# Optimization experiments

Hardware: AMD Instinct MI355X
Metric: run time of the kernel (lower is better)

## Reference

```python
import jax, jax.numpy as jnp
import numpy as np

NUM_HEADS = 12
EPS = 1e-6


def _rms_norm(x, w):
    # RMSNorm over the full channel dim (applied before head split), fp32 math
    return x * jax.lax.rsqrt(jnp.mean(x * x, axis=-1, keepdims=True) + EPS) * w


def _rope_apply(t, F, H, W, freqs):
    # t: [B, S, n, d] with S == F*H*W; freqs: [1024, d//2] angles
    B, S, n, d = t.shape
    c = d // 2
    s0 = c - 2 * (c // 3)  # temporal split (22 when d=128)
    s1 = c // 3            # spatial splits (21, 21)
    f0, f1, f2 = freqs[:, :s0], freqs[:, s0:s0 + s1], freqs[:, s0 + s1:]
    ang = jnp.concatenate([
        jnp.broadcast_to(f0[:F, None, None, :], (F, H, W, s0)),
        jnp.broadcast_to(f1[None, :H, None, :], (F, H, W, s1)),
        jnp.broadcast_to(f2[None, None, :W, :], (F, H, W, s1)),
    ], axis=-1).reshape(S, c)                      # [S, c]
    cos = jnp.cos(ang)[None, :, None, :]           # [1, S, 1, c]
    sin = jnp.sin(ang)[None, :, None, :]
    tp = t.reshape(B, S, n, c, 2)
    te, to = tp[..., 0], tp[..., 1]                # complex (real, imag) pairs
    rot = jnp.stack([te * cos - to * sin, te * sin + to * cos], axis=-1)
    return rot.reshape(B, S, n, d)


def reference(x, seq_lens, grid_sizes, freqs, Wq, bq, Wk, bk, Wv, bv, Wo, bo, norm_q_w, norm_k_w):
    B, S, C = x.shape
    n = NUM_HEADS
    d = C // n
    gs = np.asarray(grid_sizes)[0]
    F, H, W = int(gs[0]), int(gs[1]), int(gs[2])  # static: L == F*H*W, same per sample

    q = _rms_norm(x @ Wq.T + bq, norm_q_w).reshape(B, S, n, d)
    k = _rms_norm(x @ Wk.T + bk, norm_k_w).reshape(B, S, n, d)
    v = (x @ Wv.T + bv).reshape(B, S, n, d)

    q = _rope_apply(q, F, H, W, freqs)
    k = _rope_apply(k, F, H, W, freqs)

    scale = 1.0 / jnp.sqrt(jnp.float32(d))
    scores = jnp.einsum('bqnd,bknd->bnqk', q, k) * scale   # [B, n, S, S]
    kmask = jnp.arange(S)[None, :] < seq_lens[:, None]      # [B, S] valid keys
    scores = jnp.where(kmask[:, None, None, :], scores, -jnp.inf)
    attn = jax.nn.softmax(scores, axis=-1)
    out = jnp.einsum('bnqk,bknd->bqnd', attn, v).reshape(B, S, C)
    return out @ Wo.T + bo


def setup_inputs() -> dict:
    key = jax.random.key(0)
    ks = jax.random.split(key, 10)
    B, F, H, W = 2, 4, 24, 32
    S = F * H * W  # 3072
    C = 1536
    d = C // NUM_HEADS  # 128
    c = d // 2          # 64

    x = jax.random.normal(ks[0], (B, S, C), dtype=jnp.float32)
    seq_lens = jnp.array([S, 2500], dtype=jnp.int32)
    grid_sizes = jnp.array([[F, H, W]] * B, dtype=jnp.int32)

    # rope angles: outer(pos, 1/theta^(2i/dim)) per split [22, 21, 21]
    def rope_params(max_len, dim_k, theta=10000.0):
        inv = 1.0 / (theta ** (np.arange(0, dim_k, 2, dtype=np.float64) / dim_k))
        return np.outer(np.arange(max_len), inv)
    s0 = c - 2 * (c // 3)
    s1 = c // 3
    freqs = jnp.asarray(np.concatenate([
        rope_params(1024, 2 * s0), rope_params(1024, 2 * s1), rope_params(1024, 2 * s1)
    ], axis=1), dtype=jnp.float32)  # [1024, 64]

    std = 0.02
    def lin(k):
        return jax.random.normal(k, (C, C), dtype=jnp.float32) * std
    return {
        'x': x, 'seq_lens': seq_lens, 'grid_sizes': grid_sizes, 'freqs': freqs,
        'Wq': lin(ks[1]), 'bq': jnp.zeros((C,), jnp.float32),
        'Wk': lin(ks[2]), 'bk': jnp.zeros((C,), jnp.float32),
        'Wv': lin(ks[3]), 'bv': jnp.zeros((C,), jnp.float32),
        'Wo': lin(ks[4]), 'bo': jnp.zeros((C,), jnp.float32),
        'norm_q_w': jnp.ones((C,), jnp.float32),
        'norm_k_w': jnp.ones((C,), jnp.float32),
    }
```

## Files before the change

### kernel.cpp

```cpp
#include <hip/hip_runtime.h>
#include <hip/hip_bf16.h>
#include <math.h>

#define NB 2
#define SS 3072
#define CC 1536
#define NH 12
#define DH 128
#define NTOK (NB * SS)
#define WE (CC * CC)
#define LOG2E 1.4426950408889634f

typedef __attribute__((ext_vector_type(8))) short short8;
typedef __attribute__((ext_vector_type(4))) float floatx4;

#define GLOAD(g, l) __builtin_amdgcn_global_load_lds( \
    (const __attribute__((address_space(1))) void*)(g), \
    (__attribute__((address_space(3))) void*)(l), 16, 0, 0)

__device__ __forceinline__ unsigned short f2bf(float f) {
    unsigned u = __float_as_uint(f);
    u += 0x7fffu + ((u >> 16) & 1u);
    return (unsigned short)(u >> 16);
}
__device__ __forceinline__ int swz(int row, int q) {
    return row * 4 + (q ^ ((row >> 1) & 3));
}

__global__ __launch_bounds__(256) void cast_all(
    const float* __restrict__ x,
    const float* __restrict__ w0, const float* __restrict__ w1,
    const float* __restrict__ w2, const float* __restrict__ w3,
    unsigned short* __restrict__ o)
{
    const int y = blockIdx.y;
    const float* src = (y < 4) ? x + (size_t)y * WE
                     : (y == 4) ? w0 : (y == 5) ? w1 : (y == 6) ? w2 : w3;
    size_t i = ((size_t)blockIdx.x * 256 + threadIdx.x) * 4;
    float4 v = *(const float4*)&src[i];
    uint2 u;
    u.x = (unsigned)f2bf(v.x) | ((unsigned)f2bf(v.y) << 16);
    u.y = (unsigned)f2bf(v.z) | ((unsigned)f2bf(v.w) << 16);
    *(uint2*)&o[(size_t)y * WE + i] = u;
}

__global__ __launch_bounds__(256) void rope_table(
    const float* __restrict__ freqs, const int* __restrict__ gsz,
    float2* __restrict__ tab)
{
    const int id = blockIdx.x * 256 + threadIdx.x;
    const int s = id >> 6, pj = id & 63;
    const int Hg = gsz[1], Wg = gsz[2];
    const int f = s / (Hg * Wg);
    const int rem = s - f * Hg * Wg;
    const int hh = rem / Wg;
    const int ww = rem - hh * Wg;
    const int row = (pj < 22) ? f : ((pj < 43) ? hh : ww);
    float sn, cs;
    sincosf(freqs[row * 64 + pj], &sn, &cs);
    tab[id] = make_float2(cs, sn);
}

__global__ __launch_bounds__(256) void qkv_gemm(
    const unsigned short* __restrict__ X,
    const unsigned short* __restrict__ Wqb, const unsigned short* __restrict__ Wkb,
    const unsigned short* __restrict__ Wvb,
    const float* __restrict__ bq, const float* __restrict__ bk,
    const float* __restrict__ bv,
    unsigned short* __restrict__ qo, unsigned short* __restrict__ ko,
    unsigned short* __restrict__ vto)
{
    __shared__ unsigned short As[128 * 32];
    __shared__ unsigned short Bs[128 * 32];
    const int tid = threadIdx.x;
    const int w = tid >> 6, l = tid & 63;
    const int jseg = blockIdx.y / 12;
    const unsigned short* Wt = (jseg == 0) ? Wqb : (jseg == 1) ? Wkb : Wvb;
    const float* bias        = (jseg == 0) ? bq  : (jseg == 1) ? bk  : bv;
    unsigned short* Y        = (jseg == 0) ? qo  : (jseg == 1) ? ko  : vto;
    const int i0 = blockIdx.x * 128, j0 = (blockIdx.y % 12) * 128;
    const int srow = tid >> 2;
    const int gk8 = (((tid & 3) ^ ((srow >> 1) & 3))) * 8;

    floatx4 acc[4][4] = {};
    for (int k0 = 0; k0 < CC; k0 += 32) {
        __syncthreads();
        GLOAD(X + (size_t)(i0 + srow) * CC + k0 + gk8,        As + (size_t)tid * 8);
        GLOAD(X + (size_t)(i0 + 64 + srow) * CC + k0 + gk8,   As + (size_t)(256 + tid) * 8);
        GLOAD(Wt + (size_t)(j0 + srow) * CC + k0 + gk8,       Bs + (size_t)tid * 8);
        GLOAD(Wt + (size_t)(j0 + 64 + srow) * CC + k0 + gk8,  Bs + (size_t)(256 + tid) * 8);
        __syncthreads();
        const int wr = (w >> 1) * 64, wc = (w & 1) * 64;
        short8 af[4], bf[4];
        #pragma unroll
        for (int mb = 0; mb < 4; ++mb)
            af[mb] = *(const short8*)&As[swz(wr + mb * 16 + (l & 15), l >> 4) * 8];
        #pragma unroll
        for (int nb = 0; nb < 4; ++nb)
            bf[nb] = *(const short8*)&Bs[swz(wc + nb * 16 + (l & 15), l >> 4) * 8];
        #pragma unroll
        for (int mb = 0; mb < 4; ++mb)
            #pragma unroll
            for (int nb = 0; nb < 4; ++nb)
                acc[mb][nb] = __builtin_amdgcn_mfma_f32_16x16x32_bf16(
                    af[mb], bf[nb], acc[mb][nb], 0, 0, 0);
    }

    const int wr = (w >> 1) * 64, wc = (w & 1) * 64;
    #pragma unroll
    for (int mb = 0; mb < 4; ++mb)
        #pragma unroll
        for (int nb = 0; nb < 4; ++nb) {
            const int n = j0 + wc + nb * 16 + (l & 15);
            const float bv2 = bias[n];
            const int h = n >> 7, td = n & 127;
            #pragma unroll
            for (int r = 0; r < 4; ++r) {
                const int m = i0 + wr + mb * 16 + (l >> 4) * 4 + r;
                const float val = acc[mb][nb][r] + bv2;
                const int b = (m >= SS) ? 1 : 0;
                const int s = m - b * SS;
                if (jseg < 2)
                    Y[((size_t)(b * NH + h) * SS + s) * DH + td] = f2bf(val);
                else
                    Y[((size_t)(b * NH + h) * DH + td) * SS + s] = f2bf(val);
            }
        }
}

__global__ __launch_bounds__(256) void gemm_o(
    const unsigned short* __restrict__ X, const unsigned short* __restrict__ Wt,
    const float* __restrict__ bias, float* __restrict__ Y)
{
    __shared__ unsigned short As[128 * 32];
    __shared__ unsigned short Bs[128 * 32];
    const int tid = threadIdx.x;
    const int w = tid >> 6, l = tid & 63;
    const int i0 = blockIdx.x * 128, j0 = blockIdx.y * 128;
    const int srow = tid >> 2;
    const int gk8 = (((tid & 3) ^ ((srow >> 1) & 3))) * 8;

    floatx4 acc[4][4] = {};
    for (int k0 = 0; k0 < CC; k0 += 32) {
        __syncthreads();
        GLOAD(X + (size_t)(i0 + srow) * CC + k0 + gk8,        As + (size_t)tid * 8);
        GLOAD(X + (size_t)(i0 + 64 + srow) * CC + k0 + gk8,   As + (size_t)(256 + tid) * 8);
        GLOAD(Wt + (size_t)(j0 + srow) * CC + k0 + gk8,       Bs + (size_t)tid * 8);
        GLOAD(Wt + (size_t)(j0 + 64 + srow) * CC + k0 + gk8,  Bs + (size_t)(256 + tid) * 8);
        __syncthreads();
        const int wr = (w >> 1) * 64, wc = (w & 1) * 64;
        short8 af[4], bf[4];
        #pragma unroll
        for (int mb = 0; mb < 4; ++mb)
            af[mb] = *(const short8*)&As[swz(wr + mb * 16 + (l & 15), l >> 4) * 8];
        #pragma unroll
        for (int nb = 0; nb < 4; ++nb)
            bf[nb] = *(const short8*)&Bs[swz(wc + nb * 16 + (l & 15), l >> 4) * 8];
        #pragma unroll
        for (int mb = 0; mb < 4; ++mb)
            #pragma unroll
            for (int nb = 0; nb < 4; ++nb)
                acc[mb][nb] = __builtin_amdgcn_mfma_f32_16x16x32_bf16(
                    af[mb], bf[nb], acc[mb][nb], 0, 0, 0);
    }

    const int wr = (w >> 1) * 64, wc = (w & 1) * 64;
    #pragma unroll
    for (int mb = 0; mb < 4; ++mb)
        #pragma unroll
        for (int nb = 0; nb < 4; ++nb) {
            const int n = j0 + wc + nb * 16 + (l & 15);
            const float bv = bias[n];
            #pragma unroll
            for (int r = 0; r < 4; ++r) {
                const int m = i0 + wr + mb * 16 + (l >> 4) * 4 + r;
                Y[(size_t)m * CC + n] = acc[mb][nb][r] + bv;
            }
        }
}

__global__ __launch_bounds__(256) void norm_rope(
    unsigned short* __restrict__ qb, unsigned short* __restrict__ kb,
    const float* __restrict__ nqw, const float* __restrict__ nkw,
    const float2* __restrict__ tab)
{
    const int bid = blockIdx.x;
    const int which = (bid >= NTOK) ? 1 : 0;
    const int tok = bid - which * NTOK;
    unsigned short* t    = which ? kb : qb;
    const float* wgt     = which ? nkw : nqw;
    const float outscale = which ? 1.0f : 0.08838834764831845f * LOG2E;
    const int b = tok / SS, s = tok - b * SS;
    const int tid = threadIdx.x;

    float2 vals[3];
    size_t addrs[3];
    float ss = 0.f;
    #pragma unroll
    for (int kt = 0; kt < 3; ++kt) {
        int p = tid + kt * 256;
        int h = p >> 6, pj = p & 63;
        size_t addr = ((size_t)(b * NH + h) * SS + s) * DH + 2 * pj;
        addrs[kt] = addr;
        unsigned u = *(const unsigned*)&t[addr];
        float2 v;
        v.x = __uint_as_float(u << 16);
        v.y = __uint_as_float(u & 0xffff0000u);
        vals[kt] = v;
        ss += v.x * v.x + v.y * v.y;
    }
    #pragma unroll
    for (int off = 32; off > 0; off >>= 1) ss += __shfl_down(ss, off, 64);
    __shared__ float red[4];
    if ((tid & 63) == 0) red[tid >> 6] = ss;
    __syncthreads();
    const float total = red[0] + red[1] + red[2] + red[3];
    const float rstd = rsqrtf(total * (1.0f / CC) + 1e-6f) * outscale;

    #pragma unroll
    for (int kt = 0; kt < 3; ++kt) {
        int p = tid + kt * 256;
        int h = p >> 6, pj = p & 63;
        float2 cssn = tab[s * 64 + pj];
        int ch = h * DH + 2 * pj;
        float te = vals[kt].x * rstd * wgt[ch];
        float to = vals[kt].y * rstd * wgt[ch + 1];
        unsigned o = (unsigned)f2bf(te * cssn.x - to * cssn.y) |
                     ((unsigned)f2bf(te * cssn.y + to * cssn.x) << 16);
        *(unsigned*)&t[addrs[kt]] = o;
    }
}

__global__ __launch_bounds__(256, 2) void flash_attn_mfma(
    const unsigned short* __restrict__ qg, const unsigned short* __restrict__ kg,
    const unsigned short* __restrict__ vg, const int* __restrict__ seq_lens,
    unsigned short* __restrict__ out)
{
    __shared__ unsigned short lds[32768];
    const int tid = threadIdx.x;
    const int w = tid >> 6, l = tid & 63;

    const int bid = blockIdx.x;
    const int qt = bid / (NB * NH);
    const int rem0 = bid - qt * (NB * NH);
    const int h = rem0 >> 1;
    const int b = rem0 & 1;
    const int slen = seq_lens[b];
    const int s0 = qt * 128;

    const unsigned short* qbase = qg + ((size_t)(b * NH + h) * SS + s0) * DH;
    const unsigned short* kbase = kg + ((size_t)(b * NH + h) * SS) * DH;
    const unsigned short* vbase = vg + ((size_t)(b * NH + h) * DH) * SS;

    #pragma unroll
    for (int i = 0; i < 8; ++i) {
        int cid = i * 256 + tid;
        int kc = cid >> 9, r2 = cid & 511, row = r2 >> 2, sq = r2 & 3;
        GLOAD(qbase + (size_t)row * DH + kc * 32 + (sq ^ ((row >> 1) & 3)) * 8,
              lds + (size_t)cid * 8);
    }
    __syncthreads();
    short8 qf[2][4];
    #pragma unroll
    for (int rb = 0; rb < 2; ++rb)
        #pragma unroll
        for (int kc = 0; kc < 4; ++kc)
            qf[rb][kc] = *(const short8*)&lds[(kc * 512 + swz(w * 32 + rb * 16 + (l & 15), l >> 4)) * 8];
    __syncthreads();

    int ksrc[4], vsrc[4];
    #pragma unroll
    for (int i = 0; i < 4; ++i) {
        int cid = i * 256 + tid;
        {   int kc = cid >> 8, r2 = cid & 255, row = r2 >> 2, sq = r2 & 3;
            ksrc[i] = row * DH + kc * 32 + (sq ^ ((row >> 1) & 3)) * 8; }
        {   int ks = cid >> 9, r2 = cid & 511, dc = r2 >> 2, sq = r2 & 3;
            vsrc[i] = dc * SS + ks * 32 + (sq ^ ((dc >> 1) & 3)) * 8; }
    }

    const int ntiles = (slen + 63) >> 6;

    #pragma unroll
    for (int i = 0; i < 4; ++i) {
        int cid = i * 256 + tid;
        GLOAD(kbase + ksrc[i],        lds + (size_t)cid * 8);
        GLOAD(vbase + vsrc[i],        lds + 8192 + (size_t)cid * 8);
    }

    floatx4 acc[2][8] = {};
    float lsum[2] = {};
    const int g4 = (l >> 4) * 4;

    for (int kt = 0; kt < ntiles; ++kt) {
        __syncthreads();

        if (kt + 1 < ntiles) {
            const unsigned short* kb2 = kbase + (size_t)(kt + 1) * 64 * DH;
            const unsigned short* vb2 = vbase + (size_t)(kt + 1) * 64;
            unsigned short* dst = lds + ((kt + 1) & 1) * 16384;
            #pragma unroll
            for (int i = 0; i < 4; ++i) {
                int cid = i * 256 + tid;
                GLOAD(kb2 + ksrc[i], dst + (size_t)cid * 8);
                GLOAD(vb2 + vsrc[i], dst + 8192 + (size_t)cid * 8);
            }
        }

        const unsigned short* Ks = lds + (kt & 1) * 16384;
        const unsigned short* Vs = Ks + 8192;

        floatx4 sv[2][4] = {};
        __builtin_amdgcn_s_setprio(1);
        #pragma unroll
        for (int kc = 0; kc < 4; ++kc) {
            short8 kf[4];
            #pragma unroll
            for (int nb = 0; nb < 4; ++nb)
                kf[nb] = *(const short8*)&Ks[(kc * 256 + swz(nb * 16 + (l & 15), l >> 4)) * 8];
            #pragma unroll
            for (int rb = 0; rb < 2; ++rb)
                #pragma unroll
                for (int nb = 0; nb < 4; ++nb)
                    sv[rb][nb] = __builtin_amdgcn_mfma_f32_16x16x32_bf16(
                        kf[nb], qf[rb][kc], sv[rb][nb], 0, 0, 0);
        }
        __builtin_amdgcn_s_setprio(0);

        const int valid = slen - kt * 64;
        short8 pa[2][2];
        #pragma unroll
        for (int rb = 0; rb < 2; ++rb) {
            if (valid >= 64) {
                #pragma unroll
                for (int nb = 0; nb < 4; ++nb)
                    #pragma unroll
                    for (int r = 0; r < 4; ++r)
                        sv[rb][nb][r] = exp2f(sv[rb][nb][r]);
            } else {
                #pragma unroll
                for (int nb = 0; nb < 4; ++nb)
                    #pragma unroll
                    for (int r = 0; r < 4; ++r) {
                        const int key = g4 + r + 16 * nb;
                        sv[rb][nb][r] = (key < valid) ? exp2f(sv[rb][nb][r]) : 0.0f;
                    }
            }
            #pragma unroll
            for (int nb = 0; nb < 4; ++nb)
                lsum[rb] += (sv[rb][nb][0] + sv[rb][nb][1]) +
                            (sv[rb][nb][2] + sv[rb][nb][3]);

            unsigned dw0[4], dw1[4];
            #pragma unroll
            for (int nb = 0; nb < 4; ++nb) {
                union { __hip_bfloat162 v; unsigned u; } c0, c1;
                c0.v = __float22bfloat162_rn(make_float2(sv[rb][nb][0], sv[rb][nb][1]));
                c1.v = __float22bfloat162_rn(make_float2(sv[rb][nb][2], sv[rb][nb][3]));
                dw0[nb] = c0.u;
                dw1[nb] = c1.u;
            }
            #pragma unroll
            for (int ks = 0; ks < 2; ++ks) {
                unsigned x0 = dw0[2 * ks], y0 = dw0[2 * ks + 1];
                unsigned x1 = dw1[2 * ks], y1 = dw1[2 * ks + 1];
                asm("v_permlane32_swap_b32 %0, %1" : "+v"(x0), "+v"(y0));
                asm("v_permlane16_swap_b32 %0, %1" : "+v"(x0), "+v"(y0));
                asm("v_permlane32_swap_b32 %0, %1" : "+v"(x1), "+v"(y1));
                asm("v_permlane16_swap_b32 %0, %1" : "+v"(x1), "+v"(y1));
                union { short8 s; unsigned u[4]; } pk;
                pk.u[0] = x0; pk.u[1] = x1; pk.u[2] = y0; pk.u[3] = y1;
                pa[rb][ks] = pk.s;
            }
        }

        __builtin_amdgcn_s_setprio(1);
        #pragma unroll
        for (int ks = 0; ks < 2; ++ks)
            #pragma unroll
            for (int nb2 = 0; nb2 < 8; ++nb2) {
                short8 vf = *(const short8*)&Vs[(ks * 512 + swz(nb2 * 16 + (l & 15), l >> 4)) * 8];
                #pragma unroll
                for (int rb = 0; rb < 2; ++rb)
                    acc[rb][nb2] = __builtin_amdgcn_mfma_f32_16x16x32_bf16(
                        pa[rb][ks], vf, acc[rb][nb2], 0, 0, 0);
            }
        __builtin_amdgcn_s_setprio(0);
    }

    #pragma unroll
    for (int rb = 0; rb < 2; ++rb) {
        float s = lsum[rb];
        s += __shfl_xor(s, 16, 64);
        s += __shfl_xor(s, 32, 64);
        float rl[4];
        #pragma unroll
        for (int r = 0; r < 4; ++r)
            rl[r] = 1.0f / __shfl(s, g4 + r, 64);
        #pragma unroll
        for (int nb2 = 0; nb2 < 8; ++nb2) {
            const int col = h * DH + nb2 * 16 + (l & 15);
            #pragma unroll
            for (int r = 0; r < 4; ++r) {
                const int srow = s0 + w * 32 + rb * 16 + (l >> 4) * 4 + r;
                out[((size_t)b * SS + srow) * CC + col] = f2bf(acc[rb][nb2][r] * rl[r]);
            }
        }
    }
}

extern "C" void kernel_launch(void* const* d_in, const int* in_sizes, int n_in,
                              void* d_out, int out_size, void* d_ws, size_t ws_size,
                              hipStream_t stream) {
    const float* x          = (const float*)d_in[0];
    const int*   seq_lens   = (const int*)d_in[1];
    const int*   grid_sizes = (const int*)d_in[2];
    const float* freqs      = (const float*)d_in[3];
    const float* Wq         = (const float*)d_in[4];
    const float* bq         = (const float*)d_in[5];
    const float* Wk         = (const float*)d_in[6];
    const float* bk         = (const float*)d_in[7];
    const float* Wv         = (const float*)d_in[8];
    const float* bv         = (const float*)d_in[9];
    const float* Wo         = (const float*)d_in[10];
    const float* bo         = (const float*)d_in[11];
    const float* nqw        = (const float*)d_in[12];
    const float* nkw        = (const float*)d_in[13];
    float* out = (float*)d_out;

    const size_t TE = (size_t)NTOK * CC;
    unsigned short* xb  = (unsigned short*)d_ws;
    unsigned short* wqb = xb + TE;
    unsigned short* wkb = wqb + WE;
    unsigned short* wvb = wkb + WE;
    unsigned short* wob = wvb + WE;
    unsigned short* qb  = wob + WE;
    unsigned short* kb  = qb + TE;
    unsigned short* vtb = kb + TE;
    unsigned short* ab  = vtb + TE;
    float2* tab = (float2*)(ab + TE);

    cast_all<<<dim3(WE / 1024, 8), 256, 0, stream>>>(x, Wq, Wk, Wv, Wo, xb);
    rope_table<<<dim3(SS * 64 / 256), 256, 0, stream>>>(freqs, grid_sizes, tab);

    qkv_gemm<<<dim3(NTOK / 128, 36), 256, 0, stream>>>(
        xb, wqb, wkb, wvb, bq, bk, bv, qb, kb, vtb);

    norm_rope<<<dim3(2 * NTOK), 256, 0, stream>>>(qb, kb, nqw, nkw, tab);

    flash_attn_mfma<<<dim3(NB * NH * (SS / 128)), 256, 0, stream>>>(qb, kb, vtb, seq_lens, ab);

    gemm_o<<<dim3(NTOK / 128, CC / 128), 256, 0, stream>>>(ab, wob, bo, out);
}
```

Measured before the change: 519.1 us.

## Double-buffer GEMM LDS tiles and make flash attention a persistent work queue

Both GEMM kernels now double-buffer their LDS tiles. Each k-step prefetches the next tile with global_load_lds while it computes the current one, which drops one barrier per iteration. Flash attention becomes persistent: 512 blocks pull (q-tile, head, batch) items from an atomic counter that rope_table resets, which is meant to balance the uneven seq_len work. The trade-offs are more LDS per GEMM block, which may lower occupancy, plus atomic and barrier overhead per item. The GEMM prefetch also relies on the waitcnt before the single barrier for correctness.

```diff
diff --git a/kernel.cpp b/kernel.cpp
--- a/kernel.cpp
+++ b/kernel.cpp
@@ -10,6 +10,7 @@
 #define NTOK (NB * SS)
 #define WE (CC * CC)
 #define LOG2E 1.4426950408889634f
+#define NITEMS (NB * NH * (SS / 128))
 
 typedef __attribute__((ext_vector_type(8))) short short8;
 typedef __attribute__((ext_vector_type(4))) float floatx4;
@@ -46,9 +47,10 @@
 
 __global__ __launch_bounds__(256) void rope_table(
     const float* __restrict__ freqs, const int* __restrict__ gsz,
-    float2* __restrict__ tab)
+    float2* __restrict__ tab, int* __restrict__ ctr)
 {
     const int id = blockIdx.x * 256 + threadIdx.x;
+    if (id == 0) *ctr = 0;
     const int s = id >> 6, pj = id & 63;
     const int Hg = gsz[1], Wg = gsz[2];
     const int f = s / (Hg * Wg);
@@ -70,8 +72,8 @@
     unsigned short* __restrict__ qo, unsigned short* __restrict__ ko,
     unsigned short* __restrict__ vto)
 {
-    __shared__ unsigned short As[128 * 32];
-    __shared__ unsigned short Bs[128 * 32];
+    __shared__ unsigned short As[2 * 4096];
+    __shared__ unsigned short Bs[2 * 4096];
     const int tid = threadIdx.x;
     const int w = tid >> 6, l = tid & 63;
     const int jseg = blockIdx.y / 12;
@@ -82,28 +84,38 @@
     const int srow = tid >> 2;
     const int gk8 = (((tid & 3) ^ ((srow >> 1) & 3))) * 8;
 
+    GLOAD(X + (size_t)(i0 + srow) * CC + gk8,        As + (size_t)tid * 8);
+    GLOAD(X + (size_t)(i0 + 64 + srow) * CC + gk8,   As + (size_t)(256 + tid) * 8);
+    GLOAD(Wt + (size_t)(j0 + srow) * CC + gk8,       Bs + (size_t)tid * 8);
+    GLOAD(Wt + (size_t)(j0 + 64 + srow) * CC + gk8,  Bs + (size_t)(256 + tid) * 8);
+
     floatx4 acc[4][4] = {};
+    int cur = 0;
     for (int k0 = 0; k0 < CC; k0 += 32) {
         __syncthreads();
-        GLOAD(X + (size_t)(i0 + srow) * CC + k0 + gk8,        As + (size_t)tid * 8);
-        GLOAD(X + (size_t)(i0 + 64 + srow) * CC + k0 + gk8,   As + (size_t)(256 + tid) * 8);
-        GLOAD(Wt + (size_t)(j0 + srow) * CC + k0 + gk8,       Bs + (size_t)tid * 8);
-        GLOAD(Wt + (size_t)(j0 + 64 + srow) * CC + k0 + gk8,  Bs + (size_t)(256 + tid) * 8);
-        __syncthreads();
+        if (k0 + 32 < CC) {
+            const int nxt = (cur ^ 1) * 4096;
+            GLOAD(X + (size_t)(i0 + srow) * CC + k0 + 32 + gk8,        As + (size_t)(nxt + tid * 8));
+            GLOAD(X + (size_t)(i0 + 64 + srow) * CC + k0 + 32 + gk8,   As + (size_t)(nxt + (256 + tid) * 8));
+            GLOAD(Wt + (size_t)(j0 + srow) * CC + k0 + 32 + gk8,       Bs + (size_t)(nxt + tid * 8));
+            GLOAD(Wt + (size_t)(j0 + 64 + srow) * CC + k0 + 32 + gk8,  Bs + (size_t)(nxt + (256 + tid) * 8));
+        }
         const int wr = (w >> 1) * 64, wc = (w & 1) * 64;
+        const int cb = cur * 4096;
         short8 af[4], bf[4];
         #pragma unroll
         for (int mb = 0; mb < 4; ++mb)
-            af[mb] = *(const short8*)&As[swz(wr + mb * 16 + (l & 15), l >> 4) * 8];
+            af[mb] = *(const short8*)&As[cb + swz(wr + mb * 16 + (l & 15), l >> 4) * 8];
         #pragma unroll
         for (int nb = 0; nb < 4; ++nb)
-            bf[nb] = *(const short8*)&Bs[swz(wc + nb * 16 + (l & 15), l >> 4) * 8];
+            bf[nb] = *(const short8*)&Bs[cb + swz(wc + nb * 16 + (l & 15), l >> 4) * 8];
         #pragma unroll
         for (int mb = 0; mb < 4; ++mb)
             #pragma unroll
             for (int nb = 0; nb < 4; ++nb)
                 acc[mb][nb] = __builtin_amdgcn_mfma_f32_16x16x32_bf16(
                     af[mb], bf[nb], acc[mb][nb], 0, 0, 0);
+        cur ^= 1;
     }
 
     const int wr = (w >> 1) * 64, wc = (w & 1) * 64;
@@ -132,36 +144,46 @@
     const unsigned short* __restrict__ X, const unsigned short* __restrict__ Wt,
     const float* __restrict__ bias, float* __restrict__ Y)
 {
-    __shared__ unsigned short As[128 * 32];
-    __shared__ unsigned short Bs[128 * 32];
+    __shared__ unsigned short As[2 * 4096];
+    __shared__ unsigned short Bs[2 * 4096];
     const int tid = threadIdx.x;
     const int w = tid >> 6, l = tid & 63;
     const int i0 = blockIdx.x * 128, j0 = blockIdx.y * 128;
     const int srow = tid >> 2;
     const int gk8 = (((tid & 3) ^ ((srow >> 1) & 3))) * 8;
 
+    GLOAD(X + (size_t)(i0 + srow) * CC + gk8,        As + (size_t)tid * 8);
+    GLOAD(X + (size_t)(i0 + 64 + srow) * CC + gk8,   As + (size_t)(256 + tid) * 8);
+    GLOAD(Wt + (size_t)(j0 + srow) * CC + gk8,       Bs + (size_t)tid * 8);
+    GLOAD(Wt + (size_t)(j0 + 64 + srow) * CC + gk8,  Bs + (size_t)(256 + tid) * 8);
+
     floatx4 acc[4][4] = {};
+    int cur = 0;
     for (int k0 = 0; k0 < CC; k0 += 32) {
         __syncthreads();
-        GLOAD(X + (size_t)(i0 + srow) * CC + k0 + gk8,        As + (size_t)tid * 8);
-        GLOAD(X + (size_t)(i0 + 64 + srow) * CC + k0 + gk8,   As + (size_t)(256 + tid) * 8);
-        GLOAD(Wt + (size_t)(j0 + srow) * CC + k0 + gk8,       Bs + (size_t)tid * 8);
-        GLOAD(Wt + (size_t)(j0 + 64 + srow) * CC + k0 + gk8,  Bs + (size_t)(256 + tid) * 8);
-        __syncthreads();
+        if (k0 + 32 < CC) {
+            const int nxt = (cur ^ 1) * 4096;
+            GLOAD(X + (size_t)(i0 + srow) * CC + k0 + 32 + gk8,        As + (size_t)(nxt + tid * 8));
+            GLOAD(X + (size_t)(i0 + 64 + srow) * CC + k0 + 32 + gk8,   As + (size_t)(nxt + (256 + tid) * 8));
+            GLOAD(Wt + (size_t)(j0 + srow) * CC + k0 + 32 + gk8,       Bs + (size_t)(nxt + tid * 8));
+            GLOAD(Wt + (size_t)(j0 + 64 + srow) * CC + k0 + 32 + gk8,  Bs + (size_t)(nxt + (256 + tid) * 8));
+        }
         const int wr = (w >> 1) * 64, wc = (w & 1) * 64;
+        const int cb = cur * 4096;
         short8 af[4], bf[4];
         #pragma unroll
         for (int mb = 0; mb < 4; ++mb)
-            af[mb] = *(const short8*)&As[swz(wr + mb * 16 + (l & 15), l >> 4) * 8];
+            af[mb] = *(const short8*)&As[cb + swz(wr + mb * 16 + (l & 15), l >> 4) * 8];
         #pragma unroll
         for (int nb = 0; nb < 4; ++nb)
-            bf[nb] = *(const short8*)&Bs[swz(wc + nb * 16 + (l & 15), l >> 4) * 8];
+            bf[nb] = *(const short8*)&Bs[cb + swz(wc + nb * 16 + (l & 15), l >> 4) * 8];
         #pragma unroll
         for (int mb = 0; mb < 4; ++mb)
             #pragma unroll
             for (int nb = 0; nb < 4; ++nb)
                 acc[mb][nb] = __builtin_amdgcn_mfma_f32_16x16x32_bf16(
                     af[mb], bf[nb], acc[mb][nb], 0, 0, 0);
+        cur ^= 1;
     }
 
     const int wr = (w >> 1) * 64, wc = (w & 1) * 64;
@@ -234,39 +256,13 @@
 __global__ __launch_bounds__(256, 2) void flash_attn_mfma(
     const unsigned short* __restrict__ qg, const unsigned short* __restrict__ kg,
     const unsigned short* __restrict__ vg, const int* __restrict__ seq_lens,
-    unsigned short* __restrict__ out)
+    unsigned short* __restrict__ out, int* __restrict__ ctr)
 {
     __shared__ unsigned short lds[32768];
+    __shared__ int sw;
     const int tid = threadIdx.x;
     const int w = tid >> 6, l = tid & 63;
-
-    const int bid = blockIdx.x;
-    const int qt = bid / (NB * NH);
-    const int rem0 = bid - qt * (NB * NH);
-    const int h = rem0 >> 1;
-    const int b = rem0 & 1;
-    const int slen = seq_lens[b];
-    const int s0 = qt * 128;
-
-    const unsigned short* qbase = qg + ((size_t)(b * NH + h) * SS + s0) * DH;
-    const unsigned short* kbase = kg + ((size_t)(b * NH + h) * SS) * DH;
-    const unsigned short* vbase = vg + ((size_t)(b * NH + h) * DH) * SS;
-
-    #pragma unroll
-    for (int i = 0; i < 8; ++i) {
-        int cid = i * 256 + tid;
-        int kc = cid >> 9, r2 = cid & 511, row = r2 >> 2, sq = r2 & 3;
-        GLOAD(qbase + (size_t)row * DH + kc * 32 + (sq ^ ((row >> 1) & 3)) * 8,
-              lds + (size_t)cid * 8);
-    }
-    __syncthreads();
-    short8 qf[2][4];
-    #pragma unroll
-    for (int rb = 0; rb < 2; ++rb)
-        #pragma unroll
-        for (int kc = 0; kc < 4; ++kc)
-            qf[rb][kc] = *(const short8*)&lds[(kc * 512 + swz(w * 32 + rb * 16 + (l & 15), l >> 4)) * 8];
-    __syncthreads();
+    const int g4 = (l >> 4) * 4;
 
     int ksrc[4], vsrc[4];
     #pragma unroll
@@ -278,131 +274,165 @@
             vsrc[i] = dc * SS + ks * 32 + (sq ^ ((dc >> 1) & 3)) * 8; }
     }
 
-    const int ntiles = (slen + 63) >> 6;
-
-    #pragma unroll
-    for (int i = 0; i < 4; ++i) {
-        int cid = i * 256 + tid;
-        GLOAD(kbase + ksrc[i],        lds + (size_t)cid * 8);
-        GLOAD(vbase + vsrc[i],        lds + 8192 + (size_t)cid * 8);
-    }
-
-    floatx4 acc[2][8] = {};
-    float lsum[2] = {};
-    const int g4 = (l >> 4) * 4;
-
-    for (int kt = 0; kt < ntiles; ++kt) {
-        __syncthreads();
-
-        if (kt + 1 < ntiles) {
-            const unsigned short* kb2 = kbase + (size_t)(kt + 1) * 64 * DH;
-            const unsigned short* vb2 = vbase + (size_t)(kt + 1) * 64;
-            unsigned short* dst = lds + ((kt + 1) & 1) * 16384;
-            #pragma unroll
-            for (int i = 0; i < 4; ++i) {
-                int cid = i * 256 + tid;
-                GLOAD(kb2 + ksrc[i], dst + (size_t)cid * 8);
-                GLOAD(vb2 + vsrc[i], dst + 8192 + (size_t)cid * 8);
-            }
-        }
-
-        const unsigned short* Ks = lds + (kt & 1) * 16384;
-        const unsigned short* Vs = Ks + 8192;
-
-        floatx4 sv[2][4] = {};
-        __builtin_amdgcn_s_setprio(1);
-        #pragma unroll
-        for (int kc = 0; kc < 4; ++kc) {
-            short8 kf[4];
-            #pragma unroll
-            for (int nb = 0; nb < 4; ++nb)
-                kf[nb] = *(const short8*)&Ks[(kc * 256 + swz(nb * 16 + (l & 15), l >> 4)) * 8];
-            #pragma unroll
-            for (int rb = 0; rb < 2; ++rb)
+    for (;;) {
+        __syncthreads();
+        if (tid == 0) sw = atomicAdd(ctr, 1);
+        __syncthreads();
+        const int item = sw;
+        if (item >= NITEMS) break;
+
+        const int qt = item / (NB * NH);
+        const int rem0 = item - qt * (NB * NH);
+        const int h = rem0 >> 1;
+        const int b = rem0 & 1;
+        const int slen = seq_lens[b];
+        const int s0 = qt * 128;
+
+        const unsigned short* qbase = qg + ((size_t)(b * NH + h) * SS + s0) * DH;
+        const unsigned short* kbase = kg + ((size_t)(b * NH + h) * SS) * DH;
+        const unsigned short* vbase = vg + ((size_t)(b * NH + h) * DH) * SS;
+
+        #pragma unroll
+        for (int i = 0; i < 8; ++i) {
+            int cid = i * 256 + tid;
+            int kc = cid >> 9, r2 = cid & 511, row = r2 >> 2, sq = r2 & 3;
+            GLOAD(qbase + (size_t)row * DH + kc * 32 + (sq ^ ((row >> 1) & 3)) * 8,
+                  lds + (size_t)cid * 8);
+        }
+        __syncthreads();
+        short8 qf[2][4];
+        #pragma unroll
+        for (int rb = 0; rb < 2; ++rb)
+            #pragma unroll
+            for (int kc = 0; kc < 4; ++kc)
+                qf[rb][kc] = *(const short8*)&lds[(kc * 512 + swz(w * 32 + rb * 16 + (l & 15), l >> 4)) * 8];
+        __syncthreads();
+
+        const int ntiles = (slen + 63) >> 6;
+
+        #pragma unroll
+        for (int i = 0; i < 4; ++i) {
+            int cid = i * 256 + tid;
+            GLOAD(kbase + ksrc[i],        lds + (size_t)cid * 8);
+            GLOAD(vbase + vsrc[i],        lds + 8192 + (size_t)cid * 8);
+        }
+
+        floatx4 acc[2][8] = {};
+        float lsum[2] = {};
+
+        for (int kt = 0; kt < ntiles; ++kt) {
+            __syncthreads();
+
+            if (kt + 1 < ntiles) {
+                const unsigned short* kb2 = kbase + (size_t)(kt + 1) * 64 * DH;
+                const unsigned short* vb2 = vbase + (size_t)(kt + 1) * 64;
+                unsigned short* dst = lds + ((kt + 1) & 1) * 16384;
+                #pragma unroll
+                for (int i = 0; i < 4; ++i) {
+                    int cid = i * 256 + tid;
+                    GLOAD(kb2 + ksrc[i], dst + (size_t)cid * 8);
+                    GLOAD(vb2 + vsrc[i], dst + 8192 + (size_t)cid * 8);
+                }
+            }
+
+            const unsigned short* Ks = lds + (kt & 1) * 16384;
+            const unsigned short* Vs = Ks + 8192;
+
+            floatx4 sv[2][4] = {};
+            __builtin_amdgcn_s_setprio(1);
+            #pragma unroll
+            for (int kc = 0; kc < 4; ++kc) {
+                short8 kf[4];
                 #pragma unroll
                 for (int nb = 0; nb < 4; ++nb)
-                    sv[rb][nb] = __builtin_amdgcn_mfma_f32_16x16x32_bf16(
-                        kf[nb], qf[rb][kc], sv[rb][nb], 0, 0, 0);
-        }
-        __builtin_amdgcn_s_setprio(0);
-
-        const int valid = slen - kt * 64;
-        short8 pa[2][2];
+                    kf[nb] = *(const short8*)&Ks[(kc * 256 + swz(nb * 16 + (l & 15), l >> 4)) * 8];
+                #pragma unroll
+                for (int rb = 0; rb < 2; ++rb)
+                    #pragma unroll
+                    for (int nb = 0; nb < 4; ++nb)
+                        sv[rb][nb] = __builtin_amdgcn_mfma_f32_16x16x32_bf16(
+                            kf[nb], qf[rb][kc], sv[rb][nb], 0, 0, 0);
+            }
+            __builtin_amdgcn_s_setprio(0);
+
+            const int valid = slen - kt * 64;
+            short8 pa[2][2];
+            #pragma unroll
+            for (int rb = 0; rb < 2; ++rb) {
+                if (valid >= 64) {
+                    #pragma unroll
+                    for (int nb = 0; nb < 4; ++nb)
+                        #pragma unroll
+                        for (int r = 0; r < 4; ++r)
+                            sv[rb][nb][r] = exp2f(sv[rb][nb][r]);
+                } else {
+                    #pragma unroll
+                    for (int nb = 0; nb < 4; ++nb)
+                        #pragma unroll
+                        for (int r = 0; r < 4; ++r) {
+                            const int key = g4 + r + 16 * nb;
+                            sv[rb][nb][r] = (key < valid) ? exp2f(sv[rb][nb][r]) : 0.0f;
+                        }
+                }
+                #pragma unroll
+                for (int nb = 0; nb < 4; ++nb)
+                    lsum[rb] += (sv[rb][nb][0] + sv[rb][nb][1]) +
+                                (sv[rb][nb][2] + sv[rb][nb][3]);
+
+                unsigned dw0[4], dw1[4];
+                #pragma unroll
+                for (int nb = 0; nb < 4; ++nb) {
+                    union { __hip_bfloat162 v; unsigned u; } c0, c1;
+                    c0.v = __float22bfloat162_rn(make_float2(sv[rb][nb][0], sv[rb][nb][1]));
+                    c1.v = __float22bfloat162_rn(make_float2(sv[rb][nb][2], sv[rb][nb][3]));
+                    dw0[nb] = c0.u;
+                    dw1[nb] = c1.u;
+                }
+                #pragma unroll
+                for (int ks = 0; ks < 2; ++ks) {
+                    unsigned x0 = dw0[2 * ks], y0 = dw0[2 * ks + 1];
+                    unsigned x1 = dw1[2 * ks], y1 = dw1[2 * ks + 1];
+                    asm("v_permlane32_swap_b32 %0, %1" : "+v"(x0), "+v"(y0));
+                    asm("v_permlane16_swap_b32 %0, %1" : "+v"(x0), "+v"(y0));
+                    asm("v_permlane32_swap_b32 %0, %1" : "+v"(x1), "+v"(y1));
+                    asm("v_permlane16_swap_b32 %0, %1" : "+v"(x1), "+v"(y1));
+                    union { short8 s; unsigned u[4]; } pk;
+                    pk.u[0] = x0; pk.u[1] = x1; pk.u[2] = y0; pk.u[3] = y1;
+                    pa[rb][ks] = pk.s;
+                }
+            }
+
+            __builtin_amdgcn_s_setprio(1);
+            #pragma unroll
+            for (int ks = 0; ks < 2; ++ks)
+                #pragma unroll
+                for (int nb2 = 0; nb2 < 8; ++nb2) {
+                    short8 vf = *(const short8*)&Vs[(ks * 512 + swz(nb2 * 16 + (l & 15), l >> 4)) * 8];
+                    #pragma unroll
+                    for (int rb = 0; rb < 2; ++rb)
+                        acc[rb][nb2] = __builtin_amdgcn_mfma_f32_16x16x32_bf16(
+                            pa[rb][ks], vf, acc[rb][nb2], 0, 0, 0);
+                }
+            __builtin_amdgcn_s_setprio(0);
+        }
+
         #pragma unroll
         for (int rb = 0; rb < 2; ++rb) {
-            if (valid >= 64) {
-                #pragma unroll
-                for (int nb = 0; nb < 4; ++nb)
-                    #pragma unroll
-                    for (int r = 0; r < 4; ++r)
-                        sv[rb][nb][r] = exp2f(sv[rb][nb][r]);
-            } else {
-                #pragma unroll
-                for (int nb = 0; nb < 4; ++nb)
-                    #pragma unroll
-                    for (int r = 0; r < 4; ++r) {
-                        const int key = g4 + r + 16 * nb;
-                        sv[rb][nb][r] = (key < valid) ? exp2f(sv[rb][nb][r]) : 0.0f;
-                    }
-            }
-            #pragma unroll
-            for (int nb = 0; nb < 4; ++nb)
-                lsum[rb] += (sv[rb][nb][0] + sv[rb][nb][1]) +
-                            (sv[rb][nb][2] + sv[rb][nb][3]);
-
-            unsigned dw0[4], dw1[4];
-            #pragma unroll
-            for (int nb = 0; nb < 4; ++nb) {
-                union { __hip_bfloat162 v; unsigned u; } c0, c1;
-                c0.v = __float22bfloat162_rn(make_float2(sv[rb][nb][0], sv[rb][nb][1]));
-                c1.v = __float22bfloat162_rn(make_float2(sv[rb][nb][2], sv[rb][nb][3]));
-                dw0[nb] = c0.u;
-                dw1[nb] = c1.u;
-            }
-            #pragma unroll
-            for (int ks = 0; ks < 2; ++ks) {
-                unsigned x0 = dw0[2 * ks], y0 = dw0[2 * ks + 1];
-                unsigned x1 = dw1[2 * ks], y1 = dw1[2 * ks + 1];
-                asm("v_permlane32_swap_b32 %0, %1" : "+v"(x0), "+v"(y0));
-                asm("v_permlane16_swap_b32 %0, %1" : "+v"(x0), "+v"(y0));
-                asm("v_permlane32_swap_b32 %0, %1" : "+v"(x1), "+v"(y1));
-                asm("v_permlane16_swap_b32 %0, %1" : "+v"(x1), "+v"(y1));
-                union { short8 s; unsigned u[4]; } pk;
-                pk.u[0] = x0; pk.u[1] = x1; pk.u[2] = y0; pk.u[3] = y1;
-                pa[rb][ks] = pk.s;
-            }
-        }
-
-        __builtin_amdgcn_s_setprio(1);
-        #pragma unroll
-        for (int ks = 0; ks < 2; ++ks)
+            float s = lsum[rb];
+            s += __shfl_xor(s, 16, 64);
+            s += __shfl_xor(s, 32, 64);
+            float rl[4];
+            #pragma unroll
+            for (int r = 0; r < 4; ++r)
+                rl[r] = 1.0f / __shfl(s, g4 + r, 64);
             #pragma unroll
             for (int nb2 = 0; nb2 < 8; ++nb2) {
-                short8 vf = *(const short8*)&Vs[(ks * 512 + swz(nb2 * 16 + (l & 15), l >> 4)) * 8];
-                #pragma unroll
-                for (int rb = 0; rb < 2; ++rb)
-                    acc[rb][nb2] = __builtin_amdgcn_mfma_f32_16x16x32_bf16(
-                        pa[rb][ks], vf, acc[rb][nb2], 0, 0, 0);
-            }
-        __builtin_amdgcn_s_setprio(0);
-    }
-
-    #pragma unroll
-    for (int rb = 0; rb < 2; ++rb) {
-        float s = lsum[rb];
-        s += __shfl_xor(s, 16, 64);
-        s += __shfl_xor(s, 32, 64);
-        float rl[4];
-        #pragma unroll
-        for (int r = 0; r < 4; ++r)
-            rl[r] = 1.0f / __shfl(s, g4 + r, 64);
-        #pragma unroll
-        for (int nb2 = 0; nb2 < 8; ++nb2) {
-            const int col = h * DH + nb2 * 16 + (l & 15);
-            #pragma unroll
-            for (int r = 0; r < 4; ++r) {
-                const int srow = s0 + w * 32 + rb * 16 + (l >> 4) * 4 + r;
-                out[((size_t)b * SS + srow) * CC + col] = f2bf(acc[rb][nb2][r] * rl[r]);
+                const int col = h * DH + nb2 * 16 + (l & 15);
+                #pragma unroll
+                for (int r = 0; r < 4; ++r) {
+                    const int srow = s0 + w * 32 + rb * 16 + (l >> 4) * 4 + r;
+                    out[((size_t)b * SS + srow) * CC + col] = f2bf(acc[rb][nb2][r] * rl[r]);
+                }
             }
         }
     }
@@ -438,16 +468,17 @@
     unsigned short* vtb = kb + TE;
     unsigned short* ab  = vtb + TE;
     float2* tab = (float2*)(ab + TE);
+    int* ctr = (int*)(tab + (size_t)SS * 64);
 
     cast_all<<<dim3(WE / 1024, 8), 256, 0, stream>>>(x, Wq, Wk, Wv, Wo, xb);
-    rope_table<<<dim3(SS * 64 / 256), 256, 0, stream>>>(freqs, grid_sizes, tab);
+    rope_table<<<dim3(SS * 64 / 256), 256, 0, stream>>>(freqs, grid_sizes, tab, ctr);
 
     qkv_gemm<<<dim3(NTOK / 128, 36), 256, 0, stream>>>(
         xb, wqb, wkb, wvb, bq, bk, bv, qb, kb, vtb);
 
     norm_rope<<<dim3(2 * NTOK), 256, 0, stream>>>(qb, kb, nqw, nkw, tab);
 
-    flash_attn_mfma<<<dim3(NB * NH * (SS / 128)), 256, 0, stream>>>(qb, kb, vtb, seq_lens, ab);
+    flash_attn_mfma<<<dim3(512), 256, 0, stream>>>(qb, kb, vtb, seq_lens, ab, ctr);
 
     gemm_o<<<dim3(NTOK / 128, CC / 128), 256, 0, stream>>>(ab, wob, bo, out);
 }
```

After: 545.8 us. 1.05x slower.
